# Kernel optimization log

Measured on AMD Instinct MI355X. Metric: run time of the kernel, lower is better.

The kernel has to match this reference:

```python
import jax, jax.numpy as jnp
from jax import lax
import numpy as np

IMG = 512
NUM_CLASSES = 80
K_PRE = 256            # per-class pre-NMS candidates (TF combined NMS prunes similarly)
MAX_PER_CLASS = 100
MAX_TOTAL = 100
IOU_THR = 0.5
ANY_IOU_THR = 0.7
SCORE_THR = 0.05
NEG = -1e9


def make_anchors(img=IMG):
    """RetinaNet-style anchors for FPN levels 3..7, 9 per cell, [y1,x1,y2,x2]."""
    out = []
    for l in range(3, 8):
        s = 2 ** l
        n = img // s
        c = (np.arange(n) + 0.5) * s
        cy, cx = np.meshgrid(c, c, indexing='ij')
        base = 4.0 * s
        hs, ws = [], []
        for r in [0.5, 1.0, 2.0]:
            for sc in [1.0, 2 ** (1 / 3), 2 ** (2 / 3)]:
                hs.append(base * sc * np.sqrt(r))
                ws.append(base * sc / np.sqrt(r))
        hs = np.asarray(hs); ws = np.asarray(ws)  # [9]
        cy = cy[..., None]; cx = cx[..., None]
        a = np.stack([cy - hs / 2, cx - ws / 2, cy + hs / 2, cx + ws / 2], -1)  # [n,n,9,4]
        out.append(a.reshape(-1, 4))
    return np.concatenate(out, 0).astype(np.float32)


def setup_inputs() -> dict:
    key = jax.random.key(0)
    k1, k2, k3, k4 = jax.random.split(key, 4)
    anchors = jnp.asarray(make_anchors())          # [49104, 4]
    A = anchors.shape[0]
    B = 8
    # logits biased low, mimicking focal-loss bias init; few anchors fire
    y_cls = jax.random.normal(k1, (B, A, NUM_CLASSES), jnp.float32) - 4.0
    y_bbox = jax.random.normal(k2, (B, A, 4), jnp.float32) * 0.1
    orig_hs = jax.random.randint(k3, (B,), 480, 1080).astype(jnp.int32)
    orig_ws = jax.random.randint(k4, (B,), 640, 1920).astype(jnp.int32)
    return {"y_cls": y_cls, "y_bbox": y_bbox, "anchors": anchors,
            "orig_hs": orig_hs, "orig_ws": orig_ws}


def decode_boxes(anchors, rel):
    """bboxes_from_fast_rcnn: anchors [A,4], rel [B,A,4] -> [B,A,4] (y1,x1,y2,x2)."""
    ha = anchors[:, 2] - anchors[:, 0]
    wa = anchors[:, 3] - anchors[:, 1]
    cya = anchors[:, 0] + 0.5 * ha
    cxa = anchors[:, 1] + 0.5 * wa
    cy = cya + rel[..., 0] * ha
    cx = cxa + rel[..., 1] * wa
    h = ha * jnp.exp(rel[..., 2])
    w = wa * jnp.exp(rel[..., 3])
    return jnp.stack([cy - 0.5 * h, cx - 0.5 * w, cy + 0.5 * h, cx + 0.5 * w], -1)


def pairwise_iou(b):
    """[K,4] -> [K,K] IoU."""
    y1, x1, y2, x2 = b[:, 0], b[:, 1], b[:, 2], b[:, 3]
    area = (y2 - y1) * (x2 - x1)
    ih = jnp.maximum(jnp.minimum(y2[:, None], y2[None, :]) - jnp.maximum(y1[:, None], y1[None, :]), 0.0)
    iw = jnp.maximum(jnp.minimum(x2[:, None], x2[None, :]) - jnp.maximum(x1[:, None], x1[None, :]), 0.0)
    inter = ih * iw
    return inter / (area[:, None] + area[None, :] - inter + 1e-8)


def greedy_nms(boxes, valid, iou_thr, max_keep):
    """Greedy NMS over score-sorted boxes [K,4]; returns keep mask [K]."""
    K = boxes.shape[0]
    iou_m = pairwise_iou(boxes)
    ar = jnp.arange(K)

    def step(sup, i):
        k = valid[i] & jnp.logical_not(sup[i])
        sup = sup | (k & (iou_m[i] > iou_thr) & (ar > i))
        return sup, k

    _, keep = lax.scan(step, jnp.zeros(K, bool), ar)
    rank = jnp.cumsum(keep) - 1
    return keep & (rank < max_keep)


def reference(y_cls, y_bbox, anchors, orig_hs, orig_ws):
    B, A, C = y_cls.shape
    scores = jax.nn.sigmoid(y_cls)                 # [B,A,C]
    boxes = decode_boxes(anchors, y_bbox)          # [B,A,4]

    # --- per-class combined NMS ---
    st = jnp.swapaxes(scores, 1, 2)                # [B,C,A]
    top_s, top_i = lax.top_k(st, K_PRE)            # [B,C,K]
    boxes_c = jnp.take_along_axis(boxes[:, None, :, :], top_i[..., None], axis=2)  # [B,C,K,4]
    valid = top_s > SCORE_THR
    keep = jax.vmap(jax.vmap(lambda b, v: greedy_nms(b, v, IOU_THR, MAX_PER_CLASS)))(boxes_c, valid)

    masked = jnp.where(keep, top_s, NEG).reshape(B, -1)           # [B,C*K]
    cls_ids = jnp.broadcast_to(jnp.arange(C, dtype=jnp.float32)[None, :, None],
                               (B, C, K_PRE)).reshape(B, -1)
    boxes_flat = boxes_c.reshape(B, -1, 4)

    sel_s, sel_i = lax.top_k(masked, MAX_TOTAL)    # [B,T]
    sel_valid = sel_s > NEG / 2
    sel_boxes = jnp.take_along_axis(boxes_flat, sel_i[..., None], axis=1)
    sel_cls = jnp.take_along_axis(cls_ids, sel_i, axis=1)
    out_scores = jnp.where(sel_valid, sel_s, 0.0)
    out_boxes = jnp.where(sel_valid[..., None], sel_boxes, 0.0)
    out_cls = jnp.where(sel_valid, sel_cls, 0.0)
    valid_det = jnp.sum(sel_valid, axis=1).astype(jnp.int32)

    # --- resize to original image dims (bboxes_resize) ---
    rh = orig_hs.astype(jnp.float32) / IMG
    rw = orig_ws.astype(jnp.float32) / IMG
    scale = jnp.stack([rh, rw, rh, rw], -1)[:, None, :]
    lim = jnp.stack([orig_hs, orig_ws, orig_hs, orig_ws], -1).astype(jnp.float32)[:, None, :]
    rb = jnp.clip(out_boxes * scale, 0.0, lim)

    # --- class-agnostic second NMS (scores already sorted desc) ---
    v2 = jnp.arange(MAX_TOTAL)[None, :] < valid_det[:, None]
    keep2 = jax.vmap(lambda b, v: greedy_nms(b, v, ANY_IOU_THR, MAX_TOTAL))(rb, v2)

    # compact kept detections to the front (ragged gather in the original)
    perm = jnp.argsort(jnp.logical_not(keep2), axis=1, stable=True)
    fb = jnp.take_along_axis(rb, perm[..., None], axis=1)
    fs = jnp.take_along_axis(out_scores, perm, axis=1)
    fc = jnp.take_along_axis(out_cls, perm, axis=1)
    nv = jnp.sum(keep2, axis=1).astype(jnp.int32)
    m = jnp.arange(MAX_TOTAL)[None, :] < nv[:, None]
    return (jnp.where(m[..., None], fb, 0.0), jnp.where(m, fs, 0.0), jnp.where(m, fc, 0.0), nv)
```

## Files before the change

### kernel.cpp

```cpp
#include <hip/hip_runtime.h>
#include <cstdint>

#define NEGF    (-1.0e9f)
#define THR_PRE (-1.55f)
#define THR_VALID (-2.9444389791664403f)
#define CAP 512
#define FCAP 1024
#define NCLS 80
#define APB 372
#define BCAP 512
#define BLCAP 8192

__device__ __forceinline__ unsigned fkey(float v){
  unsigned b = __float_as_uint(v);
  return b ^ ((b & 0x80000000u) ? 0xFFFFFFFFu : 0x80000000u);
}
__device__ __forceinline__ float fkey_inv(unsigned k){
  unsigned b = (k & 0x80000000u) ? (k ^ 0x80000000u) : ~k;
  return __uint_as_float(b);
}
__device__ __forceinline__ int swz(int i){ return i ^ ((i >> 4) & 15); }

template<int N, int NT>
__device__ void bitonic_desc(unsigned long long* buf){
  const int tid = threadIdx.x;
  __syncthreads();
  for (int k = 2; k <= N; k <<= 1){
    for (int j = k >> 1; j > 0; j >>= 1){
      for (int t = tid; t < N/2; t += NT){
        int i = ((t & ~(j-1)) << 1) | (t & (j-1));
        int p = i | j;
        unsigned long long a = buf[i], b = buf[p];
        bool sw = ((i & k) == 0) ? (a < b) : (a > b);
        if (sw){ buf[i] = b; buf[p] = a; }
      }
      __syncthreads();
    }
  }
}

__global__ void k_init(unsigned* cnt, int n, unsigned* bcnt, int nb){
  int i = blockIdx.x*blockDim.x + threadIdx.x;
  if (i < n) cnt[i] = 0u;
  if (i < nb) bcnt[i] = 0u;
}

__global__ void k_filter(const float* __restrict__ ycls, int A,
                         unsigned* __restrict__ cnt, unsigned long long* __restrict__ pairs){
  const int b  = blockIdx.y;
  const int a0 = blockIdx.x * APB;
  const int tid = threadIdx.x;
  __shared__ unsigned long long s_cand[BCAP];
  __shared__ unsigned char     s_crow[BCAP];
  __shared__ unsigned s_n;
  __shared__ unsigned s_cnt[NCLS], s_base[NCLS], s_cur[NCLS];
  if (tid == 0) s_n = 0;
  if (tid < NCLS){ s_cnt[tid] = 0u; s_cur[tid] = 0u; }
  __syncthreads();

  const float4* p4 = (const float4*)(ycls + ((size_t)b*A + a0)*NCLS);
  const int nval = (min(APB, A - a0)) * NCLS;
  const int n4 = nval >> 2;
  for (int t = tid; t < n4; t += blockDim.x){
    float4 v = p4[t];
    int idx  = t << 2;
    int aloc = idx / NCLS;
    int c0   = idx - aloc*NCLS;
    unsigned a = (unsigned)(a0 + aloc);
    float vv[4] = {v.x, v.y, v.z, v.w};
    #pragma unroll
    for (int j = 0; j < 4; j++){
      if (vv[j] > THR_PRE){
        unsigned s = atomicAdd(&s_n, 1u);
        if (s < BCAP){
          s_cand[s] = ((unsigned long long)fkey(vv[j]) << 32) | (unsigned)(~a);
          s_crow[s] = (unsigned char)(c0 + j);
        }
      }
    }
  }
  __syncthreads();
  unsigned n = s_n; if (n > BCAP) n = BCAP;
  for (unsigned i = tid; i < n; i += blockDim.x)
    atomicAdd(&s_cnt[s_crow[i]], 1u);
  __syncthreads();
  if (tid < NCLS && s_cnt[tid] > 0u)
    s_base[tid] = atomicAdd(&cnt[b*NCLS + tid], s_cnt[tid]);
  __syncthreads();
  for (unsigned i = tid; i < n; i += blockDim.x){
    int c = s_crow[i];
    unsigned off = s_base[c] + atomicAdd(&s_cur[c], 1u);
    if (off < CAP) pairs[(size_t)(b*NCLS + c)*CAP + off] = s_cand[i];
  }
}

__global__ void k_topk_nms(const unsigned* __restrict__ cnt, const unsigned long long* __restrict__ pairs,
                           const float* __restrict__ ycls, const float4* __restrict__ ybbox,
                           const float4* __restrict__ anchors,
                           float4* __restrict__ sbox,
                           unsigned long long* __restrict__ bcand, unsigned* __restrict__ bcnt,
                           unsigned A, unsigned C){
  const int row = blockIdx.x, tid = threadIdx.x;
  const unsigned b = (unsigned)row / C, c = (unsigned)row % C;
  __shared__ __align__(16) char smem[5120];
  unsigned long long* buf = (unsigned long long*)smem;
  __shared__ unsigned s_n;
  __shared__ unsigned long long s_K;
  __shared__ unsigned long long s_keep[4];
  __shared__ unsigned s_kc, s_bbase;

  unsigned n = cnt[row]; if (n > CAP) n = CAP;
  if (n >= 256u){
    for (int i = tid; i < CAP; i += 256)
      buf[swz(i)] = (i < (int)n) ? pairs[(size_t)row*CAP + i] : 0ull;
  } else {
    if (tid == 0) s_n = 0;
    __syncthreads();
    for (int i = tid; i < CAP; i += 256) buf[swz(i)] = 0ull;
    __syncthreads();
    for (unsigned a = tid; a < A; a += 256){
      float v = ycls[((size_t)b*A + a)*C + c];
      if (v > THR_VALID){
        unsigned s = atomicAdd(&s_n, 1u);
        if (s < CAP) buf[swz(s)] = ((unsigned long long)fkey(v) << 32) | (unsigned)(~a);
      }
    }
    __syncthreads();
    n = s_n; if (n > CAP) n = CAP;
  }

  auto CE = [&](int k, int j){
    int i = ((tid & ~(j-1)) << 1) | (tid & (j-1));
    int p = i | j;
    unsigned long long a = buf[swz(i)], bb = buf[swz(p)];
    bool sw = ((i & k) == 0) ? (a < bb) : (a > bb);
    if (sw){ buf[swz(i)] = bb; buf[swz(p)] = a; }
  };
  __syncthreads();
  for (int k = 2; k <= 128; k <<= 1){
    for (int j = k >> 1; j > 0; j >>= 1){
      CE(k, j);
      __builtin_amdgcn_wave_barrier();
    }
  }
  __syncthreads();
  CE(256, 128);
  __syncthreads();
  for (int j = 64; j > 0; j >>= 1){ CE(256, j); __builtin_amdgcn_wave_barrier(); }
  __syncthreads();
  CE(512, 256);
  __syncthreads();
  CE(512, 128);
  __syncthreads();
  for (int j = 64; j > 0; j >>= 1){ CE(512, j); __builtin_amdgcn_wave_barrier(); }
  __syncthreads();

  unsigned m = n < 256u ? n : 256u;
  float lg = NEGF; float4 bx = make_float4(0.f,0.f,0.f,0.f);
  if ((unsigned)tid < m){
    unsigned long long p = buf[swz(tid)];
    unsigned key = (unsigned)(p >> 32);
    unsigned a   = ~(unsigned)(p & 0xFFFFFFFFull);
    lg = fkey_inv(key);
    float4 an = anchors[a];
    float4 rl = ybbox[(size_t)b*A + a];
    float ha = an.z - an.x, wa = an.w - an.y;
    float cya = an.x + 0.5f*ha, cxa = an.y + 0.5f*wa;
    float cy = cya + rl.x*ha, cx = cxa + rl.y*wa;
    float h = ha * expf(rl.z), w = wa * expf(rl.w);
    bx = make_float4(cy - 0.5f*h, cx - 0.5f*w, cy + 0.5f*h, cx + 0.5f*w);
  }
  sbox[(size_t)row*256 + tid] = bx;
  __syncthreads();

  float4* s_box = (float4*)smem;
  float*  s_ar  = (float*)(smem + 4096);
  float AA = (bx.z - bx.x) * (bx.w - bx.y);
  s_box[tid] = bx; s_ar[tid] = AA;
  if (tid == 0) s_kc = 0u;
  __syncthreads();

  unsigned long long M[4];
  float Y1 = bx.x, X1 = bx.y, Y2 = bx.z, X2 = bx.w;
  #pragma unroll
  for (int ch = 0; ch < 4; ++ch){
    unsigned long long mm = 0ull;
    for (int i0 = ch*64; i0 < ch*64 + 64 && i0 < tid; i0 += 4){
      #pragma unroll
      for (int k = 0; k < 4; ++k){
        int i = i0 + k;
        float4 ob = s_box[i];
        float oar = s_ar[i];
        float ih = fmaxf(fminf(Y2, ob.z) - fmaxf(Y1, ob.x), 0.f);
        float iw = fmaxf(fminf(X2, ob.w) - fmaxf(X1, ob.y), 0.f);
        float inter = ih * iw;
        float iou = inter / (AA + oar - inter + 1e-8f);
        if (iou > 0.5f && i < tid) mm |= 1ull << (i & 63);
      }
    }
    M[ch] = mm;
  }

  bool valid = lg > THR_VALID;
  bool sup = false;
  #pragma unroll
  for (int ch = 0; ch < 4; ++ch){
    __syncthreads();
    if ((tid >> 6) == ch){
      unsigned long long S = __ballot(sup);
      unsigned long long V = __ballot(valid);
      unsigned long long Mcc = M[ch];
      unsigned long long kept = 0ull, keep_o = 0ull;
      unsigned kc = s_kc;
      for (int i = 0; i < 64; ++i){
        if (((V >> i) & 1ull) && !((S >> i) & 1ull)){
          if (kc < 100u) keep_o |= 1ull << i;
          kc++;
          kept |= 1ull << i;
          S |= __ballot((Mcc >> i) & 1ull);
        }
      }
      if ((tid & 63) == 0){ s_K = kept; s_keep[ch] = keep_o; s_kc = kc; }
    }
    __syncthreads();
    sup = sup || ((M[ch] & s_K) != 0ull);
  }

  const unsigned ch4 = (unsigned)tid >> 6, ln4 = (unsigned)tid & 63u;
  bool kp = (s_keep[ch4] >> ln4) & 1ull;
  unsigned kt = (unsigned)(__popcll(s_keep[0]) + __popcll(s_keep[1]) +
                           __popcll(s_keep[2]) + __popcll(s_keep[3]));
  if (tid == 0) s_bbase = atomicAdd(&bcnt[b], kt);
  __syncthreads();
  if (kp){
    unsigned pre = (unsigned)__popcll(s_keep[ch4] & ((1ull << ln4) - 1ull));
    for (unsigned k2 = 0; k2 < ch4; ++k2) pre += (unsigned)__popcll(s_keep[k2]);
    unsigned f = c*256u + (unsigned)tid;
    bcand[(size_t)b*BLCAP + s_bbase + pre] =
      ((unsigned long long)fkey(lg) << 32) | (unsigned)(~f);
  }
}

__global__ void k_final(const unsigned long long* __restrict__ bcand, const unsigned* __restrict__ bcnt,
                        const float4* __restrict__ sbox,
                        const int* __restrict__ ohs, const int* __restrict__ ows,
                        float* __restrict__ out, int C, int B){
  const int b = blockIdx.x, tid = threadIdx.x;
  __shared__ unsigned hist[4096];
  __shared__ unsigned nb, thrkey;
  __shared__ unsigned long long buf[FCAP];
  __shared__ float ry1[100],rx1[100],ry2[100],rx2[100],rar[100],rsc[100],rcl[100];
  __shared__ unsigned long long s_K2, s_keep2[2];
  __shared__ unsigned s_kc2;

  const unsigned total = bcnt[b];
  for (int i = tid; i < 4096; i += 1024) hist[i] = 0u;
  if (tid == 0){ nb = 0u; thrkey = 0xFFFFFFFFu; s_kc2 = 0u; }
  __syncthreads();
  const unsigned long long* cb = bcand + (size_t)b*BLCAP;
  for (unsigned i = tid; i < total; i += 1024)
    atomicAdd(&hist[(unsigned)(cb[i] >> 32) >> 20], 1u);
  __syncthreads();

  const unsigned target = total < 100u ? total : 100u;
  if (tid < 64 && target > 0u){
    const int ln = tid;
    unsigned v = 0;
    #pragma unroll 8
    for (int i = 0; i < 64; i++) v += hist[(ln << 6) | ((i + ln) & 63)];
    #pragma unroll
    for (int d = 1; d < 64; d <<= 1){ unsigned u = __shfl_down(v, d); if (ln + d < 64) v += u; }
    unsigned long long gm = __ballot(v >= target);
    int gstar = 63 - __builtin_clzll(gm);
    unsigned ca = (gstar < 63) ? __shfl(v, gstar + 1) : 0u;
    unsigned h = hist[(gstar << 6) | ln];
    #pragma unroll
    for (int d = 1; d < 64; d <<= 1){ unsigned u = __shfl_down(h, d); if (ln + d < 64) h += u; }
    h += ca;
    unsigned long long bm = __ballot(h >= target);
    int bstar = 63 - __builtin_clzll(bm);
    if (ln == 0) thrkey = (unsigned)((gstar << 6) | bstar) << 20;
  }
  __syncthreads();
  const unsigned tk = thrkey;
  if (tk != 0xFFFFFFFFu){
    for (unsigned i = tid; i < total; i += 1024){
      unsigned long long e = cb[i];
      if ((unsigned)(e >> 32) >= tk){
        unsigned sl = atomicAdd(&nb, 1u);
        if (sl < FCAP) buf[sl] = e;
      }
    }
  }
  __syncthreads();
  unsigned nbv = nb; if (nbv > FCAP) nbv = FCAP;
  for (int i = tid; i < FCAP; i += 1024) if (i >= (int)nbv) buf[i] = 0ull;
  bitonic_desc<FCAP,1024>(buf);
  const int vd = (int)target;

  if (tid < 100){
    float e0=0,e1=0,e2=0,e3=0, s=0, cl=0;
    if (tid < vd){
      unsigned long long p = buf[tid];
      unsigned key = (unsigned)(p >> 32);
      unsigned f   = ~(unsigned)(p & 0xFFFFFFFFull);
      float lg = fkey_inv(key);
      s  = 1.0f / (1.0f + expf(-lg));
      int c = (int)(f >> 8), kk = (int)(f & 255u);
      cl = (float)c;
      float4 bx = sbox[((size_t)(b*C + c))*256 + kk];
      float oh = (float)ohs[b], ow = (float)ows[b];
      float rh = oh / 512.0f, rw = ow / 512.0f;
      e0 = fminf(fmaxf(bx.x*rh, 0.f), oh);
      e1 = fminf(fmaxf(bx.y*rw, 0.f), ow);
      e2 = fminf(fmaxf(bx.z*rh, 0.f), oh);
      e3 = fminf(fmaxf(bx.w*rw, 0.f), ow);
    }
    ry1[tid]=e0; rx1[tid]=e1; ry2[tid]=e2; rx2[tid]=e3;
    rar[tid]=(e2-e0)*(e3-e1); rsc[tid]=s; rcl[tid]=cl;
  }
  __syncthreads();

  unsigned long long M2[2] = {0ull, 0ull};
  if (tid < 100){
    float Y1=ry1[tid],X1=rx1[tid],Y2=ry2[tid],X2=rx2[tid],AA=rar[tid];
    for (int i = 0; i < tid; i++){
      float ih = fmaxf(fminf(Y2,ry2[i]) - fmaxf(Y1,ry1[i]), 0.f);
      float iw = fmaxf(fminf(X2,rx2[i]) - fmaxf(X1,rx1[i]), 0.f);
      float inter = ih*iw;
      float iou = inter / (AA + rar[i] - inter + 1e-8f);
      if (iou > 0.7f){ if (i < 64) M2[0] |= 1ull<<i; else M2[1] |= 1ull<<(i-64); }
    }
  }
  bool valid2 = tid < vd;
  bool sup2 = false;
  #pragma unroll
  for (int ch = 0; ch < 2; ++ch){
    __syncthreads();
    if ((tid >> 6) == ch){
      unsigned long long S = __ballot(sup2);
      unsigned long long V = __ballot(valid2);
      unsigned long long Mcc = M2[ch];
      unsigned long long kept = 0ull, keep_o = 0ull;
      unsigned kc = s_kc2;
      for (int i = 0; i < 64; ++i){
        if (((V >> i) & 1ull) && !((S >> i) & 1ull)){
          if (kc < 100u) keep_o |= 1ull << i;
          kc++;
          kept |= 1ull << i;
          S |= __ballot((Mcc >> i) & 1ull);
        }
      }
      if ((tid & 63) == 0){ s_K2 = kept; s_keep2[ch] = keep_o; s_kc2 = kc; }
    }
    __syncthreads();
    if (tid < 128) sup2 = sup2 || ((M2[ch] & s_K2) != 0ull);
  }

  float* fb  = out;
  float* fs  = out + (size_t)B*100*4;
  float* fc  = fs + (size_t)B*100;
  float* fnv = fc + (size_t)B*100;
  if (tid < 100){
    fs[b*100 + tid] = 0.f; fc[b*100 + tid] = 0.f;
    ((float4*)fb)[b*100 + tid] = make_float4(0.f,0.f,0.f,0.f);
  }
  __syncthreads();
  if (tid < 100){
    unsigned ch = (unsigned)tid >> 6, ln = (unsigned)tid & 63u;
    bool kp = (s_keep2[ch] >> ln) & 1ull;
    if (kp){
      unsigned pos = (unsigned)__popcll(s_keep2[ch] & ((1ull << ln) - 1ull));
      if (ch) pos += (unsigned)__popcll(s_keep2[0]);
      fs[b*100 + pos] = rsc[tid];
      fc[b*100 + pos] = rcl[tid];
      ((float4*)fb)[b*100 + pos] = make_float4(ry1[tid], rx1[tid], ry2[tid], rx2[tid]);
    }
  }
  if (tid == 0) fnv[b] = (float)(__popcll(s_keep2[0]) + __popcll(s_keep2[1]));
}

extern "C" void kernel_launch(void* const* d_in, const int* in_sizes, int n_in,
                              void* d_out, int out_size, void* d_ws, size_t ws_size,
                              hipStream_t stream){
  const float* ycls    = (const float*)d_in[0];
  const float* ybbox   = (const float*)d_in[1];
  const float* anchors = (const float*)d_in[2];
  const int*   ohs     = (const int*)d_in[3];
  const int*   ows     = (const int*)d_in[4];
  const int A = in_sizes[2] / 4;
  const int B = in_sizes[3];
  const int C = in_sizes[0] / (A * B);
  const int R = B * C;

  char* ws = (char*)d_ws;
  unsigned*            cnt   = (unsigned*)ws;
  unsigned long long*  pairs = (unsigned long long*)(ws + 4096);
  float4*              sbox  = (float4*)(ws + 4096 + (size_t)R*CAP*8);
  unsigned long long*  bcand = (unsigned long long*)(ws + 4096 + (size_t)R*CAP*8 + (size_t)R*256*16);
  unsigned*            bcnt  = (unsigned*)(ws + 4096 + (size_t)R*CAP*8 + (size_t)R*256*16 + (size_t)B*BLCAP*8);

  const int S = (A + APB - 1) / APB;
  k_init     <<<1, 1024, 0, stream>>>(cnt, R, bcnt, B);
  k_filter   <<<dim3(S, B), 256, 0, stream>>>(ycls, A, cnt, pairs);
  k_topk_nms <<<R, 256, 0, stream>>>(cnt, pairs, ycls, (const float4*)ybbox, (const float4*)anchors,
                                     sbox, bcand, bcnt, (unsigned)A, (unsigned)C);
  k_final    <<<B, 1024, 0, stream>>>(bcand, bcnt, sbox, ohs, ows, (float*)d_out, C, B);
}
```

Baseline: 130.1 us.

## Move per-row bitonic sort into registers with wave shuffles

Replaces the LDS-resident 512-element bitonic sort with a register-resident version. Each thread holds two elements, and compare-exchanges within a wavefront use __shfl_xor instead of shared memory loads and stores. LDS is used only for the few cross-wave stages (j=128, 256), and the swizzle helper is removed. This is meant to cut LDS traffic and bank conflicts in the top-k stage, at the cost of 64-bit shuffles, which are two 32-bit DPP/bpermute operations each.

Result: no change. 129.3 us (-0.6%).

```diff
diff --git a/kernel.cpp b/kernel.cpp
--- a/kernel.cpp
+++ b/kernel.cpp
@@ -19,7 +19,6 @@
   unsigned b = (k & 0x80000000u) ? (k ^ 0x80000000u) : ~k;
   return __uint_as_float(b);
 }
-__device__ __forceinline__ int swz(int i){ return i ^ ((i >> 4) & 15); }
 
 template<int N, int NT>
 __device__ void bitonic_desc(unsigned long long* buf){
@@ -103,67 +102,94 @@
   const int row = blockIdx.x, tid = threadIdx.x;
   const unsigned b = (unsigned)row / C, c = (unsigned)row % C;
   __shared__ __align__(16) char smem[5120];
-  unsigned long long* buf = (unsigned long long*)smem;
+  unsigned long long* L = (unsigned long long*)smem;
   __shared__ unsigned s_n;
   __shared__ unsigned long long s_K;
   __shared__ unsigned long long s_keep[4];
   __shared__ unsigned s_kc, s_bbase;
 
+  unsigned long long a, bb;
   unsigned n = cnt[row]; if (n > CAP) n = CAP;
   if (n >= 256u){
-    for (int i = tid; i < CAP; i += 256)
-      buf[swz(i)] = (i < (int)n) ? pairs[(size_t)row*CAP + i] : 0ull;
+    const unsigned long long* pr = pairs + (size_t)row*CAP;
+    int i0 = 2*tid, i1 = 2*tid + 1;
+    a  = (i0 < (int)n) ? pr[i0] : 0ull;
+    bb = (i1 < (int)n) ? pr[i1] : 0ull;
   } else {
     if (tid == 0) s_n = 0;
     __syncthreads();
-    for (int i = tid; i < CAP; i += 256) buf[swz(i)] = 0ull;
-    __syncthreads();
-    for (unsigned a = tid; a < A; a += 256){
-      float v = ycls[((size_t)b*A + a)*C + c];
+    for (int i = tid; i < CAP; i += 256) L[i] = 0ull;
+    __syncthreads();
+    for (unsigned aa = tid; aa < A; aa += 256){
+      float v = ycls[((size_t)b*A + aa)*C + c];
       if (v > THR_VALID){
         unsigned s = atomicAdd(&s_n, 1u);
-        if (s < CAP) buf[swz(s)] = ((unsigned long long)fkey(v) << 32) | (unsigned)(~a);
+        if (s < CAP) L[s] = ((unsigned long long)fkey(v) << 32) | (unsigned)(~aa);
       }
     }
     __syncthreads();
     n = s_n; if (n > CAP) n = CAP;
-  }
-
-  auto CE = [&](int k, int j){
-    int i = ((tid & ~(j-1)) << 1) | (tid & (j-1));
-    int p = i | j;
-    unsigned long long a = buf[swz(i)], bb = buf[swz(p)];
-    bool sw = ((i & k) == 0) ? (a < bb) : (a > bb);
-    if (sw){ buf[swz(i)] = bb; buf[swz(p)] = a; }
+    a = L[2*tid]; bb = L[2*tid + 1];
+    __syncthreads();
+  }
+
+  auto ce_local = [&](int k){
+    bool desc = (((2*tid) & k) == 0);
+    bool sw = desc ? (a < bb) : (a > bb);
+    if (sw){ unsigned long long t = a; a = bb; bb = t; }
   };
-  __syncthreads();
-  for (int k = 2; k <= 128; k <<= 1){
-    for (int j = k >> 1; j > 0; j >>= 1){
-      CE(k, j);
-      __builtin_amdgcn_wave_barrier();
-    }
-  }
-  __syncthreads();
-  CE(256, 128);
-  __syncthreads();
-  for (int j = 64; j > 0; j >>= 1){ CE(256, j); __builtin_amdgcn_wave_barrier(); }
-  __syncthreads();
-  CE(512, 256);
-  __syncthreads();
-  CE(512, 128);
-  __syncthreads();
-  for (int j = 64; j > 0; j >>= 1){ CE(512, j); __builtin_amdgcn_wave_barrier(); }
+  auto ce_shfl = [&](int k, int m){
+    unsigned long long pa = __shfl_xor(a, m);
+    unsigned long long pb = __shfl_xor(bb, m);
+    bool low  = ((tid & m) == 0);
+    bool desc = (((2*tid) & k) == 0);
+    bool takeMax = (low == desc);
+    a  = takeMax ? (a  > pa ? a  : pa) : (a  < pa ? a  : pa);
+    bb = takeMax ? (bb > pb ? bb : pb) : (bb < pb ? bb : pb);
+  };
+  auto ce_lds = [&](int k, int j){
+    L[2*tid] = a; L[2*tid + 1] = bb;
+    __syncthreads();
+    unsigned long long pa = L[(2*tid) ^ j];
+    unsigned long long pb = L[(2*tid + 1) ^ j];
+    bool lowa = (((2*tid) & j) == 0);
+    bool desc = (((2*tid) & k) == 0);
+    bool takeMax = (lowa == desc);
+    a  = takeMax ? (a  > pa ? a  : pa) : (a  < pa ? a  : pa);
+    bb = takeMax ? (bb > pb ? bb : pb) : (bb < pb ? bb : pb);
+    __syncthreads();
+  };
+
+  ce_local(2);
+  #pragma unroll
+  for (int k = 4; k <= 128; k <<= 1){
+    #pragma unroll
+    for (int m = k >> 2; m >= 1; m >>= 1) ce_shfl(k, m);
+    ce_local(k);
+  }
+  ce_lds(256, 128);
+  #pragma unroll
+  for (int m = 32; m >= 1; m >>= 1) ce_shfl(256, m);
+  ce_local(256);
+  ce_lds(512, 256);
+  ce_lds(512, 128);
+  #pragma unroll
+  for (int m = 32; m >= 1; m >>= 1) ce_shfl(512, m);
+  ce_local(512);
+
+  if (tid < 128){ L[2*tid] = a; L[2*tid + 1] = bb; }
+  __syncthreads();
+  unsigned long long p = L[tid];
   __syncthreads();
 
   unsigned m = n < 256u ? n : 256u;
   float lg = NEGF; float4 bx = make_float4(0.f,0.f,0.f,0.f);
   if ((unsigned)tid < m){
-    unsigned long long p = buf[swz(tid)];
     unsigned key = (unsigned)(p >> 32);
-    unsigned a   = ~(unsigned)(p & 0xFFFFFFFFull);
+    unsigned aidx = ~(unsigned)(p & 0xFFFFFFFFull);
     lg = fkey_inv(key);
-    float4 an = anchors[a];
-    float4 rl = ybbox[(size_t)b*A + a];
+    float4 an = anchors[aidx];
+    float4 rl = ybbox[(size_t)b*A + aidx];
     float ha = an.z - an.x, wa = an.w - an.y;
     float cya = an.x + 0.5f*ha, cxa = an.y + 0.5f*wa;
     float cy = cya + rl.x*ha, cx = cxa + rl.y*wa;
@@ -171,7 +197,6 @@
     bx = make_float4(cy - 0.5f*h, cx - 0.5f*w, cy + 0.5f*h, cx + 0.5f*w);
   }
   sbox[(size_t)row*256 + tid] = bx;
-  __syncthreads();
 
   float4* s_box = (float4*)smem;
   float*  s_ar  = (float*)(smem + 4096);
```
